# Performance work log

Measured on AMD Instinct MI355X. Metric: run time of the kernel, lower is better.

Reference implementation:

```python
import jax, jax.numpy as jnp
import numpy as np

N = 100000      # nodes
E = 1600000     # directed edges (before self loops)
IN_DIM = 5
HID = 64
NEG_SLOPE = 0.2  # PyG GATConv default LeakyReLU slope


def setup_inputs() -> dict:
    key = jax.random.key(0)
    ks = jax.random.split(key, 12)
    x = jax.random.normal(ks[0], (N, IN_DIM), dtype=jnp.float32)
    edge_index = jax.random.randint(ks[1], (2, E), 0, N, dtype=jnp.int64)
    # layer 1 params (GATConv(5, HID), heads=1)
    W1 = jax.random.normal(ks[2], (IN_DIM, HID), dtype=jnp.float32) * (1.0 / np.sqrt(IN_DIM))
    a_src1 = jax.random.normal(ks[3], (HID,), dtype=jnp.float32) * 0.1
    a_dst1 = jax.random.normal(ks[4], (HID,), dtype=jnp.float32) * 0.1
    b1 = jnp.zeros((HID,), dtype=jnp.float32)
    # layer 2 params (GATConv(HID, 1))
    W2 = jax.random.normal(ks[5], (HID, 1), dtype=jnp.float32) * (1.0 / np.sqrt(HID))
    a_src2 = jax.random.normal(ks[6], (1,), dtype=jnp.float32) * 0.1
    a_dst2 = jax.random.normal(ks[7], (1,), dtype=jnp.float32) * 0.1
    b2 = jnp.zeros((1,), dtype=jnp.float32)
    return {"x": x, "edge_index": edge_index,
            "W1": W1, "a_src1": a_src1, "a_dst1": a_dst1, "b1": b1,
            "W2": W2, "a_src2": a_src2, "a_dst2": a_dst2, "b2": b2}


def _gat_layer(x, W, a_src, a_dst, b, src, dst):
    h = x @ W                                   # [N, F]
    s_src = h @ a_src                           # [N] per-node src score
    s_dst = h @ a_dst                           # [N] per-node dst score
    e = s_src[src] + s_dst[dst]                 # [E'] edge logits
    e = jnp.where(e > 0, e, NEG_SLOPE * e)      # LeakyReLU(0.2)
    # segment softmax over incoming edges of each dst node
    m = jax.ops.segment_max(e, dst, num_segments=N)
    ex = jnp.exp(e - m[dst])
    denom = jax.ops.segment_sum(ex, dst, num_segments=N)
    coef = ex / denom[dst]                      # [E'] attention coefficients
    out = jax.ops.segment_sum(coef[:, None] * h[src], dst, num_segments=N)
    return out + b


def reference(x, edge_index, W1, a_src1, a_dst1, b1, W2, a_src2, a_dst2, b2):
    si = jnp.arange(N, dtype=edge_index.dtype)  # add self loops (PyG default)
    src = jnp.concatenate([edge_index[0], si])
    dst = jnp.concatenate([edge_index[1], si])
    h = _gat_layer(x, W1, a_src1, a_dst1, b1, src, dst)
    h = jax.nn.relu(h)
    return _gat_layer(h, W2, a_src2, a_dst2, b2, src, dst)  # [N, 1]
```

## Files before the change

### kernel.cpp

```cpp
#include <hip/hip_runtime.h>
#include <hip/hip_bf16.h>
#include <hip/hip_fp16.h>

#define NN 100000
#define EE 1600000
#define ET (EE + NN)
#define HID 64
#define NEG 0.2f
#define NBUK 391
#define SCT_TILE 8192
#define BUKCAP 8192

__device__ __forceinline__ float uh(unsigned u) {
    __half_raw r; r.x = (unsigned short)(u & 0xFFFF);
    return __half2float(__half(r));
}
__device__ __forceinline__ unsigned f2h(float f) {
    __half h = __float2half_rn(f);
    __half_raw r = *reinterpret_cast<__half_raw*>(&h);
    return (unsigned)r.x;
}

__global__ __launch_bounds__(256) void k_proj(const float* __restrict__ x,
                                              const float* __restrict__ W1,
                                              const float* __restrict__ a_src1,
                                              const float* __restrict__ a_dst1,
                                              unsigned* __restrict__ rec,
                                              float* __restrict__ sd1,
                                              int* __restrict__ bcur) {
    if (blockIdx.x == 0) {
        for (int i = threadIdx.x; i < 1024; i += 256) bcur[i] = 0;
    }
    int wid  = threadIdx.x >> 6;
    int lane = threadIdx.x & 63;
    int half = lane >> 5, li = lane & 31;
    int n = (blockIdx.x * 4 + wid) * 2 + half;
    if (n >= NN) return;
    float xv[5];
    float h0 = 0.f, h1 = 0.f;
#pragma unroll
    for (int k = 0; k < 5; ++k) {
        xv[k] = x[n * 5 + k];
        h0 += xv[k] * W1[k * HID + li];
        h1 += xv[k] * W1[k * HID + li + 32];
    }
    float a = h0 * a_src1[li] + h1 * a_src1[li + 32];
    float b = h0 * a_dst1[li] + h1 * a_dst1[li + 32];
#pragma unroll
    for (int o = 1; o <= 16; o <<= 1) { a += __shfl_xor(a, o); b += __shfl_xor(b, o); }
    if (li == 0) {
        sd1[n] = b;
        uint4 rv;
        rv.x = __float_as_uint(a);
        rv.y = f2h(xv[0]) | (f2h(xv[1]) << 16);
        rv.z = f2h(xv[2]) | (f2h(xv[3]) << 16);
        rv.w = f2h(xv[4]);
        *(uint4*)(rec + (size_t)n * 4) = rv;
    }
}

__global__ __launch_bounds__(1024) void k_bscatter(const int* __restrict__ ei,
                                                   int* __restrict__ bcur,
                                                   unsigned* __restrict__ pairs) {
    __shared__ unsigned sp[SCT_TILE];
    __shared__ unsigned short bid[SCT_TILE];
    __shared__ int cnt_[NBUK], loc[NBUK], cur[NBUK];
    __shared__ int wsum[16];
    int tid = threadIdx.x;
    int wid = tid >> 6, lane = tid & 63;
    int base = blockIdx.x * SCT_TILE;
    int tilecnt = ET - base; if (tilecnt > SCT_TILE) tilecnt = SCT_TILE;

    for (int i = tid; i < NBUK; i += 1024) cnt_[i] = 0;
    __syncthreads();
    int sreg[8], dreg[8], rreg[8];
#pragma unroll
    for (int it = 0; it < 2; ++it) {
        int i = base + (it * 1024 + tid) * 4;
        if (i + 3 < EE) {
            const int4 sv = *(const int4*)(ei + i);
            const int4 dv = *(const int4*)(ei + EE + i);
            sreg[it*4+0] = sv.x; sreg[it*4+1] = sv.y; sreg[it*4+2] = sv.z; sreg[it*4+3] = sv.w;
            dreg[it*4+0] = dv.x; dreg[it*4+1] = dv.y; dreg[it*4+2] = dv.z; dreg[it*4+3] = dv.w;
        } else {
#pragma unroll
            for (int k = 0; k < 4; ++k) {
                int idx = i + k;
                if (idx < EE)      { sreg[it*4+k] = ei[idx];  dreg[it*4+k] = ei[EE + idx]; }
                else if (idx < ET) { sreg[it*4+k] = idx - EE; dreg[it*4+k] = idx - EE; }
                else               { dreg[it*4+k] = -1; }
            }
        }
#pragma unroll
        for (int k = 0; k < 4; ++k)
            if (dreg[it*4+k] >= 0) rreg[it*4+k] = atomicAdd(&cnt_[dreg[it*4+k] >> 8], 1);
    }
    __syncthreads();
    int b0 = tid * 4;
    int s0 = 0;
    if (b0 < NBUK)
        for (int k = 0; k < 4 && b0 + k < NBUK; ++k) s0 += cnt_[b0 + k];
    int incl = s0;
#pragma unroll
    for (int o = 1; o < 64; o <<= 1) {
        int t = __shfl(incl, (lane - o) & 63);
        if (lane >= o) incl += t;
    }
    if (lane == 63) wsum[wid] = incl;
    __syncthreads();
    int wpref = 0;
    for (int w = 0; w < wid; ++w) wpref += wsum[w];
    if (b0 < NBUK) {
        int run = wpref + incl - s0;
        for (int k = 0; k < 4 && b0 + k < NBUK; ++k) {
            loc[b0 + k] = run;
            run += cnt_[b0 + k];
        }
    }
    __syncthreads();
    for (int i = tid; i < NBUK; i += 1024) {
        int c = cnt_[i];
        cur[i] = c ? (atomicAdd(&bcur[i], c) + i * BUKCAP - loc[i]) : 0;
    }
    __syncthreads();
#pragma unroll
    for (int q = 0; q < 8; ++q) {
        if (dreg[q] >= 0) {
            int s = sreg[q], d = dreg[q];
            int b = d >> 8;
            int slot = loc[b] + rreg[q];
            sp[slot]  = ((unsigned)(d & 255) << 17) | (unsigned)s;
            bid[slot] = (unsigned short)b;
        }
    }
    __syncthreads();
    for (int i = tid; i < tilecnt; i += 1024)
        pairs[cur[bid[i]] + i] = sp[i];
}

__global__ __launch_bounds__(1024) void k_bsort(const int* __restrict__ bcur,
                                                unsigned* __restrict__ pairs,
                                                int* __restrict__ rowptr,
                                                int* __restrict__ cntd) {
    __shared__ int hist[256], sc[256];
    int b = blockIdx.x;
    int cnt = bcur[b];
    if (cnt > BUKCAP) cnt = BUKCAP;
    int base = b * BUKCAP;
    int tid = threadIdx.x;
    if (tid < 256) hist[tid] = 0;
    __syncthreads();
    unsigned preg[8];
    int rreg[8];
    int i0 = tid * 8;
    if (i0 + 8 <= cnt) {
        const uint4 v0 = *(const uint4*)(pairs + base + i0);
        const uint4 v1 = *(const uint4*)(pairs + base + i0 + 4);
        preg[0] = v0.x; preg[1] = v0.y; preg[2] = v0.z; preg[3] = v0.w;
        preg[4] = v1.x; preg[5] = v1.y; preg[6] = v1.z; preg[7] = v1.w;
    } else {
#pragma unroll
        for (int j = 0; j < 8; ++j)
            preg[j] = (i0 + j < cnt) ? pairs[base + i0 + j] : 0xFFFFFFFFu;
    }
#pragma unroll
    for (int j = 0; j < 8; ++j)
        if (preg[j] != 0xFFFFFFFFu) rreg[j] = atomicAdd(&hist[preg[j] >> 17], 1);
    __syncthreads();
    if (tid < 64) {
        int v0 = hist[4 * tid], v1 = hist[4 * tid + 1];
        int v2 = hist[4 * tid + 2], v3 = hist[4 * tid + 3];
        int s = v0 + v1 + v2 + v3;
#pragma unroll
        for (int o = 1; o < 64; o <<= 1) {
            int t = __shfl(s, (tid - o) & 63);
            if (tid >= o) s += t;
        }
        int excl = s - v0 - v1 - v2 - v3;
        sc[4 * tid]     = excl;
        sc[4 * tid + 1] = excl + v0;
        sc[4 * tid + 2] = excl + v0 + v1;
        sc[4 * tid + 3] = excl + v0 + v1 + v2;
    }
    __syncthreads();
    int nbase = b << 8;
    if (tid < 256 && nbase + tid < NN) {
        rowptr[nbase + tid] = base + sc[tid];
        cntd[nbase + tid]   = hist[tid];
    }
    int* adj = (int*)pairs;
#pragma unroll
    for (int j = 0; j < 8; ++j) {
        if (preg[j] != 0xFFFFFFFFu) {
            int ld = (int)(preg[j] >> 17);
            adj[base + sc[ld] + rreg[j]] = (int)(preg[j] & 0x1FFFF);
        }
    }
}

__device__ __forceinline__ void agg1_node_gen(int n, int lane,
                                              const int* __restrict__ rowptr,
                                              const int* __restrict__ cntd,
                                              const int* __restrict__ adj,
                                              const unsigned* __restrict__ rec,
                                              const float* __restrict__ sd1,
                                              const float* __restrict__ W1,
                                              const float* __restrict__ b1,
                                              const float* __restrict__ W2,
                                              float* __restrict__ h2) {
    int off = rowptr[n], deg = cntd[n];
    float sdn = sd1[n];
    float dsum = 0.f, a0 = 0.f, a1 = 0.f, a2 = 0.f, a3 = 0.f, a4 = 0.f;
    for (int j0 = 0; j0 < deg; j0 += 64) {
        int j = j0 + lane;
        if (j < deg) {
            int s = adj[off + j];
            const uint4 v = *(const uint4*)(rec + (size_t)s * 4);
            float t = __uint_as_float(v.x) + sdn;
            float e = t > 0.f ? t : NEG * t;
            float w = __expf(e);
            dsum += w;
            a0 += w * uh(v.y); a1 += w * uh(v.y >> 16);
            a2 += w * uh(v.z); a3 += w * uh(v.z >> 16);
            a4 += w * uh(v.w);
        }
    }
#pragma unroll
    for (int o = 32; o; o >>= 1) {
        dsum += __shfl_xor(dsum, o);
        a0 += __shfl_xor(a0, o); a1 += __shfl_xor(a1, o); a2 += __shfl_xor(a2, o);
        a3 += __shfl_xor(a3, o); a4 += __shfl_xor(a4, o);
    }
    float inv = 1.0f / dsum;
    a0 *= inv; a1 *= inv; a2 *= inv; a3 *= inv; a4 *= inv;
    float of = b1[lane] + a0 * W1[lane] + a1 * W1[64 + lane] + a2 * W1[128 + lane]
             + a3 * W1[192 + lane] + a4 * W1[256 + lane];
    of = fmaxf(of, 0.f);
    float p2 = of * W2[lane];
#pragma unroll
    for (int o = 32; o; o >>= 1) p2 += __shfl_xor(p2, o);
    if (lane == 0) h2[n] = p2;
}

__global__ __launch_bounds__(256) void k_agg1(const int* __restrict__ rowptr,
                                              const int* __restrict__ cntd,
                                              const int* __restrict__ adj,
                                              const unsigned* __restrict__ rec,
                                              const float* __restrict__ sd1,
                                              const float* __restrict__ W1,
                                              const float* __restrict__ b1,
                                              const float* __restrict__ W2,
                                              float* __restrict__ h2) {
    int wid  = threadIdx.x >> 6;
    int lane = threadIdx.x & 63;
    int n0 = (blockIdx.x * 4 + wid) * 2;
    if (n0 >= NN) return;
    int d0 = cntd[n0], d1 = cntd[n0 + 1];

    if (d0 <= 32 && d1 <= 32) {
        int half = lane >> 5, li = lane & 31;
        int n = n0 + half;
        int off = rowptr[n];
        int deg = half ? d1 : d0;
        float sdn = sd1[n];
        int s = adj[off + (li < deg ? li : 0)];
        const uint4 v = *(const uint4*)(rec + (size_t)s * 4);
        float t = __uint_as_float(v.x) + sdn;
        float e = t > 0.f ? t : NEG * t;
        float p = (li < deg) ? __expf(e) : 0.f;
        float ds = p;
        float a0 = p * uh(v.y), a1 = p * uh(v.y >> 16);
        float a2 = p * uh(v.z), a3 = p * uh(v.z >> 16);
        float a4 = p * uh(v.w);
#pragma unroll
        for (int o = 1; o <= 16; o <<= 1) {
            ds += __shfl_xor(ds, o);
            a0 += __shfl_xor(a0, o); a1 += __shfl_xor(a1, o); a2 += __shfl_xor(a2, o);
            a3 += __shfl_xor(a3, o); a4 += __shfl_xor(a4, o);
        }
        float inv = 1.0f / ds;
        a0 *= inv; a1 *= inv; a2 *= inv; a3 *= inv; a4 *= inv;
        float o0 = b1[li] + a0 * W1[li] + a1 * W1[64 + li] + a2 * W1[128 + li]
                 + a3 * W1[192 + li] + a4 * W1[256 + li];
        float o1 = b1[li + 32] + a0 * W1[li + 32] + a1 * W1[96 + li] + a2 * W1[160 + li]
                 + a3 * W1[224 + li] + a4 * W1[288 + li];
        o0 = fmaxf(o0, 0.f);
        o1 = fmaxf(o1, 0.f);
        float p2 = o0 * W2[li] + o1 * W2[li + 32];
#pragma unroll
        for (int o = 1; o <= 16; o <<= 1) p2 += __shfl_xor(p2, o);
        if (li == 0) h2[n] = p2;
    } else {
        agg1_node_gen(n0,     lane, rowptr, cntd, adj, rec, sd1, W1, b1, W2, h2);
        agg1_node_gen(n0 + 1, lane, rowptr, cntd, adj, rec, sd1, W1, b1, W2, h2);
    }
}

__device__ __forceinline__ void agg2_node(int n, int lane,
                                          const int* __restrict__ rowptr,
                                          const int* __restrict__ cntd,
                                          const int* __restrict__ adj,
                                          const float* __restrict__ h2,
                                          float as2v, float ad2v, float b2v,
                                          float* __restrict__ out) {
    int off = rowptr[n], deg = cntd[n];
    float sdn = h2[n] * ad2v;
    float dsum = 0.f, nsum = 0.f;
    for (int j0 = 0; j0 < deg; j0 += 64) {
        int j = j0 + lane;
        if (j < deg) {
            int s = adj[off + j];
            float hv = h2[s];
            float e = hv * as2v + sdn;
            e = e > 0.f ? e : NEG * e;
            float ex = __expf(e);
            dsum += ex;
            nsum += ex * hv;
        }
    }
#pragma unroll
    for (int o = 32; o; o >>= 1) { dsum += __shfl_xor(dsum, o); nsum += __shfl_xor(nsum, o); }
    if (lane == 0) out[n] = nsum / dsum + b2v;
}

__global__ __launch_bounds__(256) void k_agg2(const int* __restrict__ rowptr,
                                              const int* __restrict__ cntd,
                                              const int* __restrict__ adj,
                                              const float* __restrict__ h2,
                                              const float* __restrict__ as2,
                                              const float* __restrict__ ad2,
                                              const float* __restrict__ b2,
                                              float* __restrict__ out) {
    int wid  = threadIdx.x >> 6;
    int lane = threadIdx.x & 63;
    int n0 = (blockIdx.x * 4 + wid) * 4;
    if (n0 >= NN) return;
    float as2v = as2[0], ad2v = ad2[0], b2v = b2[0];
    int d0 = cntd[n0], d1 = cntd[n0 + 1], d2 = cntd[n0 + 2], d3 = cntd[n0 + 3];

    if (d0 <= 32 && d1 <= 32 && d2 <= 32 && d3 <= 32) {
        int half = lane >> 5, li = lane & 31;
        int nA = n0 + half, nB = n0 + 2 + half;
        int offA = rowptr[nA], offB = rowptr[nB];
        int degA = half ? d1 : d0, degB = half ? d3 : d2;
        float sdA = h2[nA] * ad2v, sdB = h2[nB] * ad2v;
        float hvA = 0.f, hvB = 0.f, pA = 0.f, pB = 0.f;
        if (li < degA) {
            hvA = h2[adj[offA + li]];
            float t = hvA * as2v + sdA;
            pA = __expf(t > 0.f ? t : NEG * t);
        }
        if (li < degB) {
            hvB = h2[adj[offB + li]];
            float t = hvB * as2v + sdB;
            pB = __expf(t > 0.f ? t : NEG * t);
        }
        float dsA = pA, dsB = pB, nsA = pA * hvA, nsB = pB * hvB;
#pragma unroll
        for (int o = 1; o <= 16; o <<= 1) {
            dsA += __shfl_xor(dsA, o); nsA += __shfl_xor(nsA, o);
            dsB += __shfl_xor(dsB, o); nsB += __shfl_xor(nsB, o);
        }
        if (li == 0) {
            out[nA] = nsA / dsA + b2v;
            out[nB] = nsB / dsB + b2v;
        }
    } else {
        agg2_node(n0,     lane, rowptr, cntd, adj, h2, as2v, ad2v, b2v, out);
        agg2_node(n0 + 1, lane, rowptr, cntd, adj, h2, as2v, ad2v, b2v, out);
        agg2_node(n0 + 2, lane, rowptr, cntd, adj, h2, as2v, ad2v, b2v, out);
        agg2_node(n0 + 3, lane, rowptr, cntd, adj, h2, as2v, ad2v, b2v, out);
    }
}

extern "C" void kernel_launch(void* const* d_in, const int* in_sizes, int n_in,
                              void* d_out, int out_size, void* d_ws, size_t ws_size,
                              hipStream_t stream) {
    const float* x      = (const float*)d_in[0];
    const int*   ei     = (const int*)d_in[1];
    const float* W1     = (const float*)d_in[2];
    const float* a_src1 = (const float*)d_in[3];
    const float* a_dst1 = (const float*)d_in[4];
    const float* b1     = (const float*)d_in[5];
    const float* W2     = (const float*)d_in[6];
    const float* as2    = (const float*)d_in[7];
    const float* ad2    = (const float*)d_in[8];
    const float* b2     = (const float*)d_in[9];
    float* out = (float*)d_out;

    unsigned* rec = (unsigned*)d_ws;
    float* sd1  = (float*)(rec + (size_t)NN * 4);
    float* h2   = sd1 + NN;
    int* rowptr = (int*)(h2 + NN);
    int* cntd   = rowptr + NN;
    int* bcur   = cntd + NN;
    unsigned* pairs = (unsigned*)(bcur + 1024);
    int* adj    = (int*)pairs;

    const int NSCT = (ET + SCT_TILE - 1) / SCT_TILE;
    const int NPROJ = (NN / 2 + 3) / 4;
    const int NPAIR = (NN / 2 + 3) / 4;
    const int NQUAD = (NN + 15) / 16;

    k_proj<<<NPROJ, 256, 0, stream>>>(x, W1, a_src1, a_dst1, rec, sd1, bcur);
    k_bscatter<<<NSCT, 1024, 0, stream>>>(ei, bcur, pairs);
    k_bsort<<<NBUK, 1024, 0, stream>>>(bcur, pairs, rowptr, cntd);
    k_agg1<<<NPAIR, 256, 0, stream>>>(rowptr, cntd, adj, rec, sd1, W1, b1, W2, h2);
    k_agg2<<<NQUAD, 256, 0, stream>>>(rowptr, cntd, adj, h2, as2, ad2, b2, out);
}
```

Baseline: 77.41 us.

## Merge projection into scatter kernel and interleave rowptr/degree arrays

The separate projection kernel is folded into the bucket-scatter kernel as extra blocks, so the two independent front stages run in one launch. The bucket counter reset moves to a memset. Row offsets and degrees are stored as interleaved int2 pairs, so the aggregation kernels fetch both with one vector load instead of two scattered loads. The cost is heavyweight 1024-thread blocks with large shared memory for the projection work, plus an extra memset call.

```diff
diff --git a/kernel.cpp b/kernel.cpp
--- a/kernel.cpp
+++ b/kernel.cpp
@@ -21,52 +21,54 @@
     return (unsigned)r.x;
 }
 
-__global__ __launch_bounds__(256) void k_proj(const float* __restrict__ x,
-                                              const float* __restrict__ W1,
-                                              const float* __restrict__ a_src1,
-                                              const float* __restrict__ a_dst1,
-                                              unsigned* __restrict__ rec,
-                                              float* __restrict__ sd1,
-                                              int* __restrict__ bcur) {
-    if (blockIdx.x == 0) {
-        for (int i = threadIdx.x; i < 1024; i += 256) bcur[i] = 0;
-    }
-    int wid  = threadIdx.x >> 6;
-    int lane = threadIdx.x & 63;
-    int half = lane >> 5, li = lane & 31;
-    int n = (blockIdx.x * 4 + wid) * 2 + half;
-    if (n >= NN) return;
-    float xv[5];
-    float h0 = 0.f, h1 = 0.f;
-#pragma unroll
-    for (int k = 0; k < 5; ++k) {
-        xv[k] = x[n * 5 + k];
-        h0 += xv[k] * W1[k * HID + li];
-        h1 += xv[k] * W1[k * HID + li + 32];
-    }
-    float a = h0 * a_src1[li] + h1 * a_src1[li + 32];
-    float b = h0 * a_dst1[li] + h1 * a_dst1[li + 32];
-#pragma unroll
-    for (int o = 1; o <= 16; o <<= 1) { a += __shfl_xor(a, o); b += __shfl_xor(b, o); }
-    if (li == 0) {
-        sd1[n] = b;
-        uint4 rv;
-        rv.x = __float_as_uint(a);
-        rv.y = f2h(xv[0]) | (f2h(xv[1]) << 16);
-        rv.z = f2h(xv[2]) | (f2h(xv[3]) << 16);
-        rv.w = f2h(xv[4]);
-        *(uint4*)(rec + (size_t)n * 4) = rv;
-    }
-}
-
-__global__ __launch_bounds__(1024) void k_bscatter(const int* __restrict__ ei,
-                                                   int* __restrict__ bcur,
-                                                   unsigned* __restrict__ pairs) {
+#define NSCT ((ET + SCT_TILE - 1) / SCT_TILE)
+#define NPROJB ((NN + 31) / 32)
+
+__global__ __launch_bounds__(1024) void k_front(const float* __restrict__ x,
+                                                const float* __restrict__ W1,
+                                                const float* __restrict__ a_src1,
+                                                const float* __restrict__ a_dst1,
+                                                const int* __restrict__ ei,
+                                                unsigned* __restrict__ rec,
+                                                float* __restrict__ sd1,
+                                                int* __restrict__ bcur,
+                                                unsigned* __restrict__ pairs) {
     __shared__ unsigned sp[SCT_TILE];
     __shared__ unsigned short bid[SCT_TILE];
     __shared__ int cnt_[NBUK], loc[NBUK], cur[NBUK];
     __shared__ int wsum[16];
     int tid = threadIdx.x;
+
+    if (blockIdx.x >= NSCT) {
+        int p = blockIdx.x - NSCT;
+        int wid  = tid >> 6;
+        int half = (tid >> 5) & 1, li = tid & 31;
+        int n = p * 32 + wid * 2 + half;
+        if (n >= NN) return;
+        float xv[5];
+        float h0 = 0.f, h1 = 0.f;
+#pragma unroll
+        for (int k = 0; k < 5; ++k) {
+            xv[k] = x[n * 5 + k];
+            h0 += xv[k] * W1[k * HID + li];
+            h1 += xv[k] * W1[k * HID + li + 32];
+        }
+        float a = h0 * a_src1[li] + h1 * a_src1[li + 32];
+        float b = h0 * a_dst1[li] + h1 * a_dst1[li + 32];
+#pragma unroll
+        for (int o = 1; o <= 16; o <<= 1) { a += __shfl_xor(a, o); b += __shfl_xor(b, o); }
+        if (li == 0) {
+            sd1[n] = b;
+            uint4 rv;
+            rv.x = __float_as_uint(a);
+            rv.y = f2h(xv[0]) | (f2h(xv[1]) << 16);
+            rv.z = f2h(xv[2]) | (f2h(xv[3]) << 16);
+            rv.w = f2h(xv[4]);
+            *(uint4*)(rec + (size_t)n * 4) = rv;
+        }
+        return;
+    }
+
     int wid = tid >> 6, lane = tid & 63;
     int base = blockIdx.x * SCT_TILE;
     int tilecnt = ET - base; if (tilecnt > SCT_TILE) tilecnt = SCT_TILE;
@@ -140,8 +142,7 @@
 
 __global__ __launch_bounds__(1024) void k_bsort(const int* __restrict__ bcur,
                                                 unsigned* __restrict__ pairs,
-                                                int* __restrict__ rowptr,
-                                                int* __restrict__ cntd) {
+                                                int2* __restrict__ rowcnt) {
     __shared__ int hist[256], sc[256];
     int b = blockIdx.x;
     int cnt = bcur[b];
@@ -184,10 +185,8 @@
     }
     __syncthreads();
     int nbase = b << 8;
-    if (tid < 256 && nbase + tid < NN) {
-        rowptr[nbase + tid] = base + sc[tid];
-        cntd[nbase + tid]   = hist[tid];
-    }
+    if (tid < 256 && nbase + tid < NN)
+        rowcnt[nbase + tid] = make_int2(base + sc[tid], hist[tid]);
     int* adj = (int*)pairs;
 #pragma unroll
     for (int j = 0; j < 8; ++j) {
@@ -198,9 +197,7 @@
     }
 }
 
-__device__ __forceinline__ void agg1_node_gen(int n, int lane,
-                                              const int* __restrict__ rowptr,
-                                              const int* __restrict__ cntd,
+__device__ __forceinline__ void agg1_node_gen(int n, int lane, int off, int deg,
                                               const int* __restrict__ adj,
                                               const unsigned* __restrict__ rec,
                                               const float* __restrict__ sd1,
@@ -208,7 +205,6 @@
                                               const float* __restrict__ b1,
                                               const float* __restrict__ W2,
                                               float* __restrict__ h2) {
-    int off = rowptr[n], deg = cntd[n];
     float sdn = sd1[n];
     float dsum = 0.f, a0 = 0.f, a1 = 0.f, a2 = 0.f, a3 = 0.f, a4 = 0.f;
     for (int j0 = 0; j0 < deg; j0 += 64) {
@@ -242,8 +238,7 @@
     if (lane == 0) h2[n] = p2;
 }
 
-__global__ __launch_bounds__(256) void k_agg1(const int* __restrict__ rowptr,
-                                              const int* __restrict__ cntd,
+__global__ __launch_bounds__(256) void k_agg1(const int* __restrict__ rowcnt,
                                               const int* __restrict__ adj,
                                               const unsigned* __restrict__ rec,
                                               const float* __restrict__ sd1,
@@ -255,12 +250,13 @@
     int lane = threadIdx.x & 63;
     int n0 = (blockIdx.x * 4 + wid) * 2;
     if (n0 >= NN) return;
-    int d0 = cntd[n0], d1 = cntd[n0 + 1];
+    const int4 rc = *(const int4*)(rowcnt + n0 * 2);
+    int off0 = rc.x, d0 = rc.y, off1 = rc.z, d1 = rc.w;
 
     if (d0 <= 32 && d1 <= 32) {
         int half = lane >> 5, li = lane & 31;
         int n = n0 + half;
-        int off = rowptr[n];
+        int off = half ? off1 : off0;
         int deg = half ? d1 : d0;
         float sdn = sd1[n];
         int s = adj[off + (li < deg ? li : 0)];
@@ -291,19 +287,16 @@
         for (int o = 1; o <= 16; o <<= 1) p2 += __shfl_xor(p2, o);
         if (li == 0) h2[n] = p2;
     } else {
-        agg1_node_gen(n0,     lane, rowptr, cntd, adj, rec, sd1, W1, b1, W2, h2);
-        agg1_node_gen(n0 + 1, lane, rowptr, cntd, adj, rec, sd1, W1, b1, W2, h2);
-    }
-}
-
-__device__ __forceinline__ void agg2_node(int n, int lane,
-                                          const int* __restrict__ rowptr,
-                                          const int* __restrict__ cntd,
+        agg1_node_gen(n0,     lane, off0, d0, adj, rec, sd1, W1, b1, W2, h2);
+        agg1_node_gen(n0 + 1, lane, off1, d1, adj, rec, sd1, W1, b1, W2, h2);
+    }
+}
+
+__device__ __forceinline__ void agg2_node(int n, int lane, int off, int deg,
                                           const int* __restrict__ adj,
                                           const float* __restrict__ h2,
                                           float as2v, float ad2v, float b2v,
                                           float* __restrict__ out) {
-    int off = rowptr[n], deg = cntd[n];
     float sdn = h2[n] * ad2v;
     float dsum = 0.f, nsum = 0.f;
     for (int j0 = 0; j0 < deg; j0 += 64) {
@@ -323,8 +316,7 @@
     if (lane == 0) out[n] = nsum / dsum + b2v;
 }
 
-__global__ __launch_bounds__(256) void k_agg2(const int* __restrict__ rowptr,
-                                              const int* __restrict__ cntd,
+__global__ __launch_bounds__(256) void k_agg2(const int* __restrict__ rowcnt,
                                               const int* __restrict__ adj,
                                               const float* __restrict__ h2,
                                               const float* __restrict__ as2,
@@ -336,12 +328,15 @@
     int n0 = (blockIdx.x * 4 + wid) * 4;
     if (n0 >= NN) return;
     float as2v = as2[0], ad2v = ad2[0], b2v = b2[0];
-    int d0 = cntd[n0], d1 = cntd[n0 + 1], d2 = cntd[n0 + 2], d3 = cntd[n0 + 3];
+    const int4 rcA = *(const int4*)(rowcnt + n0 * 2);
+    const int4 rcB = *(const int4*)(rowcnt + n0 * 2 + 4);
+    int d0 = rcA.y, d1 = rcA.w, d2 = rcB.y, d3 = rcB.w;
 
     if (d0 <= 32 && d1 <= 32 && d2 <= 32 && d3 <= 32) {
         int half = lane >> 5, li = lane & 31;
         int nA = n0 + half, nB = n0 + 2 + half;
-        int offA = rowptr[nA], offB = rowptr[nB];
+        int offA = half ? rcA.z : rcA.x;
+        int offB = half ? rcB.z : rcB.x;
         int degA = half ? d1 : d0, degB = half ? d3 : d2;
         float sdA = h2[nA] * ad2v, sdB = h2[nB] * ad2v;
         float hvA = 0.f, hvB = 0.f, pA = 0.f, pB = 0.f;
@@ -366,10 +361,10 @@
             out[nB] = nsB / dsB + b2v;
         }
     } else {
-        agg2_node(n0,     lane, rowptr, cntd, adj, h2, as2v, ad2v, b2v, out);
-        agg2_node(n0 + 1, lane, rowptr, cntd, adj, h2, as2v, ad2v, b2v, out);
-        agg2_node(n0 + 2, lane, rowptr, cntd, adj, h2, as2v, ad2v, b2v, out);
-        agg2_node(n0 + 3, lane, rowptr, cntd, adj, h2, as2v, ad2v, b2v, out);
+        agg2_node(n0,     lane, rcA.x, d0, adj, h2, as2v, ad2v, b2v, out);
+        agg2_node(n0 + 1, lane, rcA.z, d1, adj, h2, as2v, ad2v, b2v, out);
+        agg2_node(n0 + 2, lane, rcB.x, d2, adj, h2, as2v, ad2v, b2v, out);
+        agg2_node(n0 + 3, lane, rcB.z, d3, adj, h2, as2v, ad2v, b2v, out);
     }
 }
 
@@ -391,20 +386,18 @@
     unsigned* rec = (unsigned*)d_ws;
     float* sd1  = (float*)(rec + (size_t)NN * 4);
     float* h2   = sd1 + NN;
-    int* rowptr = (int*)(h2 + NN);
-    int* cntd   = rowptr + NN;
-    int* bcur   = cntd + NN;
+    int2* rowcnt = (int2*)(h2 + NN);
+    int* bcur   = (int*)(rowcnt + NN);
     unsigned* pairs = (unsigned*)(bcur + 1024);
     int* adj    = (int*)pairs;
 
-    const int NSCT = (ET + SCT_TILE - 1) / SCT_TILE;
-    const int NPROJ = (NN / 2 + 3) / 4;
     const int NPAIR = (NN / 2 + 3) / 4;
     const int NQUAD = (NN + 15) / 16;
 
-    k_proj<<<NPROJ, 256, 0, stream>>>(x, W1, a_src1, a_dst1, rec, sd1, bcur);
-    k_bscatter<<<NSCT, 1024, 0, stream>>>(ei, bcur, pairs);
-    k_bsort<<<NBUK, 1024, 0, stream>>>(bcur, pairs, rowptr, cntd);
-    k_agg1<<<NPAIR, 256, 0, stream>>>(rowptr, cntd, adj, rec, sd1, W1, b1, W2, h2);
-    k_agg2<<<NQUAD, 256, 0, stream>>>(rowptr, cntd, adj, h2, as2, ad2, b2, out);
-}
+    hipMemsetAsync(bcur, 0, 1024 * sizeof(int), stream);
+    k_front<<<NSCT + NPROJB, 1024, 0, stream>>>(x, W1, a_src1, a_dst1, ei,
+                                                rec, sd1, bcur, pairs);
+    k_bsort<<<NBUK, 1024, 0, stream>>>(bcur, pairs, rowcnt);
+    k_agg1<<<NPAIR, 256, 0, stream>>>((const int*)rowcnt, adj, rec, sd1, W1, b1, W2, h2);
+    k_agg2<<<NQUAD, 256, 0, stream>>>((const int*)rowcnt, adj, h2, as2, ad2, b2, out);
+}
```

Measured after the change: 76.30 us. No clear change (-1.4%).
